# Optimization experiments

Hardware: AMD Instinct MI355X
Metric: run time of the kernel (lower is better)

## Reference

```python
import jax, jax.numpy as jnp
import numpy as np

N = 20000
E = 320000
IN_CH = 512
OUT_CH = 256


def setup_inputs() -> dict:
    key = jax.random.key(0)
    ks = jax.random.split(key, 24)
    p = lambda k, shape: jax.random.normal(k, shape, jnp.float32) * 0.05
    return {
        "x": jax.random.normal(ks[0], (N, IN_CH), jnp.float32),
        "edge_index": jax.random.randint(ks[1], (2, E), 0, N),
        "original_size": 16384,
        "W1": p(ks[2], (IN_CH, 4 * 256)), "as1": p(ks[3], (4, 256)), "ad1": p(ks[4], (4, 256)), "b1": p(ks[5], (1024,)),
        "lw1": p(ks[6], (IN_CH, 1024)), "lb1": p(ks[7], (1024,)),
        "W2": p(ks[8], (1024, 4 * 256)), "as2": p(ks[9], (4, 256)), "ad2": p(ks[10], (4, 256)), "b2": p(ks[11], (1024,)),
        "lw2": p(ks[12], (1024, 1024)), "lb2": p(ks[13], (1024,)),
        "W3": p(ks[14], (1024, 6 * 256)), "as3": p(ks[15], (6, 256)), "ad3": p(ks[16], (6, 256)), "b3": p(ks[17], (256,)),
        "lw3": p(ks[18], (1024, OUT_CH)), "lb3": p(ks[19], (OUT_CH,)),
    }


def gat_conv(x, src, dst, W, a_src, a_dst, bias, heads, ch, concat):
    """PyG-style GATConv: gather -> edge attention -> segment softmax -> scatter-add."""
    n = x.shape[0]
    h = (x @ W).reshape(n, heads, ch)                      # [N,H,C]
    alpha_s = (h * a_src[None]).sum(-1)                    # [N,H]
    alpha_d = (h * a_dst[None]).sum(-1)                    # [N,H]
    e = jax.nn.leaky_relu(alpha_s[src] + alpha_d[dst], 0.2)  # [E,H]
    m = jax.ops.segment_max(e, dst, num_segments=n)        # per-dst max (stable softmax)
    e = jnp.exp(e - m[dst])
    denom = jax.ops.segment_sum(e, dst, num_segments=n)
    alpha = e / (denom[dst] + 1e-16)                       # [E,H]
    msg = h[src] * alpha[:, :, None]                       # [E,H,C]
    out = jax.ops.segment_sum(msg, dst, num_segments=n)    # [N,H,C]
    out = out.reshape(n, heads * ch) if concat else out.mean(axis=1)
    return out + bias


def reference(x, edge_index, original_size, W1, as1, ad1, b1, lw1, lb1,
              W2, as2, ad2, b2, lw2, lb2, W3, as3, ad3, b3, lw3, lb3):
    n = x.shape[0]
    loops = jnp.arange(n)
    src = jnp.concatenate([edge_index[0], loops])  # PyG add_self_loops=True default
    dst = jnp.concatenate([edge_index[1], loops])
    h = jax.nn.elu(gat_conv(x, src, dst, W1, as1, ad1, b1, 4, 256, True) + x @ lw1 + lb1)
    h = jax.nn.elu(gat_conv(h, src, dst, W2, as2, ad2, b2, 4, 256, True) + h @ lw2 + lb2)
    h = gat_conv(h, src, dst, W3, as3, ad3, b3, 6, 256, False) + h @ lw3 + lb3
    return h[:original_size]
```

## Files before the change

kernel.cpp:

```cpp
#include <hip/hip_runtime.h>

#define N_NODES 20000
#define M_PAD   20096
#define E_EDGES 320000

typedef unsigned short u16;
typedef unsigned int   u32;
typedef __attribute__((ext_vector_type(8))) short bf16x8;
typedef __attribute__((ext_vector_type(4))) float f32x4;
typedef __attribute__((ext_vector_type(4))) u32   u32x4;

__device__ __forceinline__ float bf2f(u16 u){
  u32 x = ((u32)u) << 16; float f; __builtin_memcpy(&f, &x, 4); return f;
}
__device__ __forceinline__ u16 f2bf(float f){
  u32 u; __builtin_memcpy(&u, &f, 4);
  u += 0x7fffu + ((u >> 16) & 1u);
  return (u16)(u >> 16);
}
__device__ __forceinline__ float lrelu(float x){ return x > 0.f ? x : 0.2f * x; }

__device__ __forceinline__ void gl_lds16(const void* g, void* l){
  __builtin_amdgcn_global_load_lds((const __attribute__((address_space(1))) void*)g,
                                   (__attribute__((address_space(3))) void*)l, 16, 0, 0);
}

__device__ __forceinline__ void acc8(float* acc, float w, u32x4 p){
#pragma unroll
  for (int d = 0; d < 4; d++){
    u32 u = p[d];
    acc[2 * d]     += w * bf2f((u16)(u & 0xffff));
    acc[2 * d + 1] += w * bf2f((u16)(u >> 16));
  }
}

__device__ __forceinline__ void acc24(float* acc, float w0, float w1, int bnd,
                                      u32x4 p0, u32x4 p1, u32x4 p2){
  u32 u[12];
  *(u32x4*)(u) = p0; *(u32x4*)(u + 4) = p1; *(u32x4*)(u + 8) = p2;
#pragma unroll
  for (int d = 0; d < 12; d++){
    float w = (2 * d < bnd) ? w0 : w1;
    acc[2 * d]     += w * bf2f((u16)(u[d] & 0xffff));
    acc[2 * d + 1] += w * bf2f((u16)(u[d] >> 16));
  }
}

__device__ __forceinline__ float sel6(const float* a, int h){
  float r = a[0];
  r = (h == 1) ? a[1] : r; r = (h == 2) ? a[2] : r; r = (h == 3) ? a[3] : r;
  r = (h == 4) ? a[4] : r; r = (h == 5) ? a[5] : r;
  return r;
}

__global__ void hist_k(const int* __restrict__ ei, int* __restrict__ cnt){
  int i = blockIdx.x * 256 + threadIdx.x;
  if (i < E_EDGES) atomicAdd(&cnt[ei[E_EDGES + i]], 1);
}

__global__ void scan_k(const int* __restrict__ cnt, int* __restrict__ rowp,
                       int* __restrict__ fill, int n){
  __shared__ int wsum[16], wpre[16];
  __shared__ int carry;
  int tid = threadIdx.x, lane = tid & 63, wv = tid >> 6;
  if (tid == 0) carry = 0;
  __syncthreads();
  for (int base = 0; base < n; base += 1024){
    int i = base + tid;
    int v = (i < n) ? cnt[i] : 0;
    int incl = v;
#pragma unroll
    for (int d = 1; d < 64; d <<= 1){
      int t = __shfl_up(incl, d, 64);
      if (lane >= d) incl += t;
    }
    if (lane == 63) wsum[wv] = incl;
    __syncthreads();
    if (tid == 0){
      int s = carry;
#pragma unroll
      for (int w = 0; w < 16; w++){ wpre[w] = s; s += wsum[w]; }
      carry = s;
    }
    __syncthreads();
    if (i < n){ int e = wpre[wv] + incl - v; rowp[i] = e; fill[i] = e; }
  }
  __syncthreads();
  if (tid == 0) rowp[n] = carry;
}

__global__ void scatter_k(const int* __restrict__ ei, int* __restrict__ fill, int* __restrict__ esrc){
  int i = blockIdx.x * 256 + threadIdx.x;
  if (i < E_EDGES){
    int d = ei[E_EDGES + i];
    int p = atomicAdd(&fill[d], 1);
    esrc[p] = ei[i];
  }
}

__global__ void tcast_all(const float* __restrict__ W1, const float* __restrict__ lw1, u16* __restrict__ Wt1,
                          const float* __restrict__ W2, const float* __restrict__ lw2, u16* __restrict__ Wt2,
                          const float* __restrict__ W3, const float* __restrict__ lw3, u16* __restrict__ Wt3)
{
  __shared__ float tile[32][33];
  int b = blockIdx.x;
  const float* src; u16* dst; int Nc, n0, ldd;
  if      (b <  512){            src = W1;  Nc = 1024; dst = Wt1; n0 = 0;    ldd = 512;  }
  else if (b < 1024){ b -=  512; src = lw1; Nc = 1024; dst = Wt1; n0 = 1024; ldd = 512;  }
  else if (b < 2048){ b -= 1024; src = W2;  Nc = 1024; dst = Wt2; n0 = 0;    ldd = 1024; }
  else if (b < 3072){ b -= 2048; src = lw2; Nc = 1024; dst = Wt2; n0 = 1024; ldd = 1024; }
  else if (b < 4608){ b -= 3072; src = W3;  Nc = 1536; dst = Wt3; n0 = 0;    ldd = 1024; }
  else              { b -= 4608; src = lw3; Nc = 256;  dst = Wt3; n0 = 1536; ldd = 1024; }
  int gx = Nc / 32;
  int kb = (b / gx) * 32, nb = (b % gx) * 32;
  int tx = threadIdx.x, ty = threadIdx.y;
#pragma unroll
  for (int r = 0; r < 32; r += 8)
    tile[ty + r][tx] = src[(size_t)(kb + ty + r) * Nc + nb + tx];
  __syncthreads();
#pragma unroll
  for (int r = 0; r < 32; r += 8){
    int n = nb + ty + r;
    dst[(size_t)(n0 + n) * ldd + kb + tx] = f2bf(tile[tx][ty + r]);
  }
}

__global__ void castx_k(const float* __restrict__ x, u16* __restrict__ o, int realRows){
  int r = blockIdx.x, c = threadIdx.x * 2;
  float2 v = (r < realRows) ? *(const float2*)(x + (size_t)r * 512 + c) : make_float2(0.f, 0.f);
  u32 pk = ((u32)f2bf(v.y) << 16) | (u32)f2bf(v.x);
  *(u32*)(o + (size_t)r * 512 + c) = pk;
}

__global__ void zpad_k(u16* __restrict__ p, int n){
  int i = blockIdx.x * 256 + threadIdx.x; if (i < n) p[i] = 0;
}

__global__ __launch_bounds__(256, 2)
void gemm_bf16(const u16* __restrict__ A, const u16* __restrict__ Bt, u16* __restrict__ C,
               int N, int K,
               const float* __restrict__ a_s, const float* __restrict__ a_d,
               float* __restrict__ aS, float* __restrict__ aD, int H)
{
  __shared__ __attribute__((aligned(16))) u16 lA[128 * 32];
  __shared__ __attribute__((aligned(16))) u16 lB[256 * 32];
  const int tid  = threadIdx.x;
  const int wave = tid >> 6, lane = tid & 63;
  const int bn = blockIdx.x, bm = blockIdx.y;
  const int wm = (wave >> 1) * 64, wn = (wave & 1) * 128;

  const int srow  = wave * 16 + (lane >> 2);
  const int skcol = (lane & 3) * 8;
  const u16* Ag0 = A  + (size_t)(bm * 128 + srow) * K + skcol;
  const u16* Ag1 = Ag0 + (size_t)64 * K;
  const u16* Bg  = Bt + (size_t)(bn * 256 + srow) * K + skcol;
  u16* lA0 = lA + wave * 512; u16* lA1 = lA + 2048 + wave * 512;
  u16* lBw = lB + wave * 512;

  f32x4 acc[4][8] = {};

  for (int k0 = 0; k0 < K; k0 += 32){
    gl_lds16(Ag0 + k0, lA0);
    gl_lds16(Ag1 + k0, lA1);
#pragma unroll
    for (int c = 0; c < 4; c++)
      gl_lds16(Bg + (size_t)(c * 64) * K + k0, lBw + c * 2048);
    __syncthreads();
    const int koff = (lane >> 4) * 8;
    const int rsel = lane & 15;
    bf16x8 af[4], bfr[8];
#pragma unroll
    for (int i = 0; i < 4; i++) af[i]  = *(const bf16x8*)&lA[(wm + i * 16 + rsel) * 32 + koff];
#pragma unroll
    for (int j = 0; j < 8; j++) bfr[j] = *(const bf16x8*)&lB[(wn + j * 16 + rsel) * 32 + koff];
#pragma unroll
    for (int i = 0; i < 4; i++)
#pragma unroll
      for (int j = 0; j < 8; j++)
        acc[i][j] = __builtin_amdgcn_mfma_f32_16x16x32_bf16(af[i], bfr[j], acc[i][j], 0, 0, 0);
    __syncthreads();
  }

  const int r0 = (lane >> 4) * 4, cl = lane & 15;
#pragma unroll
  for (int i = 0; i < 4; i++)
#pragma unroll
    for (int j = 0; j < 8; j++){
      int row = bm * 128 + wm + i * 16 + r0;
      int col = bn * 256 + wn + j * 16 + cl;
      u16* cp = C + (size_t)row * N + col;
#pragma unroll
      for (int r = 0; r < 4; r++) cp[(size_t)r * N] = f2bf(acc[i][j][r]);
    }

  if (bn < H){
    float* fa = (float*)lA;
    fa[tid]       = a_s[bn * 256 + tid];
    fa[256 + tid] = a_d[bn * 256 + tid];
    __syncthreads();
    float* fb = (float*)lB;
    const int q = lane >> 4;
#pragma unroll
    for (int i = 0; i < 4; i++)
#pragma unroll
      for (int r = 0; r < 4; r++){
        float ps = 0.f, pd = 0.f;
#pragma unroll
        for (int j = 0; j < 8; j++){
          float v = acc[i][j][r];
          int c = wn + j * 16 + cl;
          ps += v * fa[c];
          pd += v * fa[256 + c];
        }
#pragma unroll
        for (int m = 1; m < 16; m <<= 1){
          ps += __shfl_xor(ps, m, 64);
          pd += __shfl_xor(pd, m, 64);
        }
        if (cl == 0){
          int row = wm + i * 16 + q * 4 + r;
          fb[(wave & 1) * 128 + row]       = ps;
          fb[256 + (wave & 1) * 128 + row] = pd;
        }
      }
    __syncthreads();
    if (tid < 128){
      int row = bm * 128 + tid;
      aS[(size_t)row * 8 + bn] = fb[tid] + fb[128 + tid];
      aD[(size_t)row * 8 + bn] = fb[256 + tid] + fb[384 + tid];
    }
  }
}

__global__ __launch_bounds__(256)
void agg4w_k(const u16* __restrict__ HG, int ldH,
             const int* __restrict__ rowp, const int* __restrict__ esrc,
             const float* __restrict__ aS, const float* __restrict__ aD,
             const float* __restrict__ bias, const float* __restrict__ lbias,
             u16* __restrict__ outb)
{
  __shared__ float s_w[4][256];
  const int tid = threadIdx.x, lane = tid & 63, wv = tid >> 6;
  const int dst = blockIdx.x * 4 + wv;
  const int e0 = rowp[dst];
  const int deg = rowp[dst + 1] - e0;
  const int nE = deg + 1;
  const float4 adv = *(const float4*)(aD + (size_t)dst * 8);

  int myS = dst;
  float ea = -1e30f, eb = -1e30f, ec = -1e30f, ed = -1e30f;
  if (lane < nE){
    myS = (lane == deg) ? dst : esrc[e0 + lane];
    float4 as = *(const float4*)(aS + (size_t)myS * 8);
    ea = lrelu(as.x + adv.x); eb = lrelu(as.y + adv.y);
    ec = lrelu(as.z + adv.z); ed = lrelu(as.w + adv.w);
  }
  float m0 = ea, m1 = eb, m2 = ec, m3 = ed;
  for (int i = lane + 64; i < nE; i += 64){
    int s = (i == deg) ? dst : esrc[e0 + i];
    float4 as = *(const float4*)(aS + (size_t)s * 8);
    m0 = fmaxf(m0, lrelu(as.x + adv.x)); m1 = fmaxf(m1, lrelu(as.y + adv.y));
    m2 = fmaxf(m2, lrelu(as.z + adv.z)); m3 = fmaxf(m3, lrelu(as.w + adv.w));
  }
#pragma unroll
  for (int off = 1; off < 64; off <<= 1){
    m0 = fmaxf(m0, __shfl_xor(m0, off)); m1 = fmaxf(m1, __shfl_xor(m1, off));
    m2 = fmaxf(m2, __shfl_xor(m2, off)); m3 = fmaxf(m3, __shfl_xor(m3, off));
  }

  float w0 = __expf(ea - m0), w1 = __expf(eb - m1);
  float w2 = __expf(ec - m2), w3 = __expf(ed - m3);
  float l0 = w0, l1 = w1, l2 = w2, l3 = w3;
  for (int i = lane + 64; i < nE; i += 64){
    int s = (i == deg) ? dst : esrc[e0 + i];
    float4 as = *(const float4*)(aS + (size_t)s * 8);
    l0 += __expf(lrelu(as.x + adv.x) - m0); l1 += __expf(lrelu(as.y + adv.y) - m1);
    l2 += __expf(lrelu(as.z + adv.z) - m2); l3 += __expf(lrelu(as.w + adv.w) - m3);
  }
#pragma unroll
  for (int off = 1; off < 64; off <<= 1){
    l0 += __shfl_xor(l0, off); l1 += __shfl_xor(l1, off);
    l2 += __shfl_xor(l2, off); l3 += __shfl_xor(l3, off);
  }
  float d0 = 1.f / (l0 + 1e-16f), d1 = 1.f / (l1 + 1e-16f);
  float d2 = 1.f / (l2 + 1e-16f), d3 = 1.f / (l3 + 1e-16f);
  *(float4*)&s_w[wv][lane * 4] = make_float4(w0 * d0, w1 * d1, w2 * d2, w3 * d3);
  __syncthreads();

  const int h = lane >> 4;
  const int ch0 = lane * 16;
  const float mh   = (h < 2) ? (h == 0 ? m0 : m1) : (h == 2 ? m2 : m3);
  const float dh   = (h < 2) ? (h == 0 ? d0 : d1) : (h == 2 ? d2 : d3);
  const float advh = (h < 2) ? (h == 0 ? adv.x : adv.y) : (h == 2 ? adv.z : adv.w);
  float acc[16] = {};
  const u16* HGc = HG + ch0;
  const int nF = nE < 64 ? nE : 64;
  int i = 0;
  for (; i + 1 < nF; i += 2){
    int sA = __shfl(myS, i), sB = __shfl(myS, i + 1);
    float wA = s_w[wv][i * 4 + h], wB = s_w[wv][(i + 1) * 4 + h];
    const u16* ra = HGc + (size_t)sA * ldH;
    const u16* rb = HGc + (size_t)sB * ldH;
    u32x4 pa0 = *(const u32x4*)ra, pa1 = *(const u32x4*)(ra + 8);
    u32x4 pb0 = *(const u32x4*)rb, pb1 = *(const u32x4*)(rb + 8);
    acc8(acc, wA, pa0); acc8(acc + 8, wA, pa1);
    acc8(acc, wB, pb0); acc8(acc + 8, wB, pb1);
  }
  if (i < nF){
    int sA = __shfl(myS, i);
    float wA = s_w[wv][i * 4 + h];
    const u16* ra = HGc + (size_t)sA * ldH;
    acc8(acc, wA, *(const u32x4*)ra); acc8(acc + 8, wA, *(const u32x4*)(ra + 8));
  }
  for (int j = 64; j < nE; j++){
    int s = (j == deg) ? dst : esrc[e0 + j];
    float e = lrelu(aS[(size_t)s * 8 + h] + advh);
    float w = __expf(e - mh) * dh;
    const u16* r = HGc + (size_t)s * ldH;
    acc8(acc, w, *(const u32x4*)r); acc8(acc + 8, w, *(const u32x4*)(r + 8));
  }

  const u16* lr = HG + (size_t)dst * ldH + 1024 + ch0;
  u32x4 q0 = *(const u32x4*)lr, q1 = *(const u32x4*)(lr + 8);
  float lin[16];
#pragma unroll
  for (int d = 0; d < 4; d++){
    lin[2*d]     = bf2f((u16)(q0[d] & 0xffff)); lin[2*d+1]   = bf2f((u16)(q0[d] >> 16));
    lin[8+2*d]   = bf2f((u16)(q1[d] & 0xffff)); lin[8+2*d+1] = bf2f((u16)(q1[d] >> 16));
  }
  u32 o[8];
#pragma unroll
  for (int d = 0; d < 8; d++){
    float va = acc[2*d]   + bias[ch0 + 2*d]   + lin[2*d]   + lbias[ch0 + 2*d];
    float vb = acc[2*d+1] + bias[ch0 + 2*d+1] + lin[2*d+1] + lbias[ch0 + 2*d+1];
    va = va > 0.f ? va : __expf(va) - 1.f;
    vb = vb > 0.f ? vb : __expf(vb) - 1.f;
    o[d] = ((u32)f2bf(vb) << 16) | (u32)f2bf(va);
  }
  u16* op = outb + (size_t)dst * 1024 + ch0;
  *(u32x4*)op = *(u32x4*)o;
  *(u32x4*)(op + 8) = *(u32x4*)(o + 4);
}

__global__ __launch_bounds__(256)
void agg6w_k(const u16* __restrict__ HG, int ldH,
             const int* __restrict__ rowp, const int* __restrict__ esrc,
             const float* __restrict__ aS, const float* __restrict__ aD,
             const float* __restrict__ bias, const float* __restrict__ lbias,
             float* __restrict__ outf)
{
  __shared__ float s_w[4][64 * 6];
  __shared__ float s_fin[4][1536];
  const int tid = threadIdx.x, lane = tid & 63, wv = tid >> 6;
  const int dst = blockIdx.x * 4 + wv;
  const int e0 = rowp[dst];
  const int deg = rowp[dst + 1] - e0;
  const int nE = deg + 1;

  const float* advp = aD + (size_t)dst * 8;
  float4 av4 = *(const float4*)advp; float2 av2 = *(const float2*)(advp + 4);
  float adv[6] = { av4.x, av4.y, av4.z, av4.w, av2.x, av2.y };

  int myS = dst;
  float e[6];
#pragma unroll
  for (int h = 0; h < 6; h++) e[h] = -1e30f;
  if (lane < nE){
    myS = (lane == deg) ? dst : esrc[e0 + lane];
    float4 a0 = *(const float4*)(aS + (size_t)myS * 8);
    float2 a1 = *(const float2*)(aS + (size_t)myS * 8 + 4);
    e[0] = lrelu(a0.x + adv[0]); e[1] = lrelu(a0.y + adv[1]);
    e[2] = lrelu(a0.z + adv[2]); e[3] = lrelu(a0.w + adv[3]);
    e[4] = lrelu(a1.x + adv[4]); e[5] = lrelu(a1.y + adv[5]);
  }
  float m[6];
#pragma unroll
  for (int h = 0; h < 6; h++) m[h] = e[h];
  for (int i = lane + 64; i < nE; i += 64){
    int s = (i == deg) ? dst : esrc[e0 + i];
    float4 a0 = *(const float4*)(aS + (size_t)s * 8);
    float2 a1 = *(const float2*)(aS + (size_t)s * 8 + 4);
    float t[6] = { a0.x, a0.y, a0.z, a0.w, a1.x, a1.y };
#pragma unroll
    for (int h = 0; h < 6; h++) m[h] = fmaxf(m[h], lrelu(t[h] + adv[h]));
  }
#pragma unroll
  for (int h = 0; h < 6; h++)
#pragma unroll
    for (int off = 1; off < 64; off <<= 1) m[h] = fmaxf(m[h], __shfl_xor(m[h], off));

  float w[6], l[6];
#pragma unroll
  for (int h = 0; h < 6; h++){ w[h] = __expf(e[h] - m[h]); l[h] = w[h]; }
  for (int i = lane + 64; i < nE; i += 64){
    int s = (i == deg) ? dst : esrc[e0 + i];
    float4 a0 = *(const float4*)(aS + (size_t)s * 8);
    float2 a1 = *(const float2*)(aS + (size_t)s * 8 + 4);
    float t[6] = { a0.x, a0.y, a0.z, a0.w, a1.x, a1.y };
#pragma unroll
    for (int h = 0; h < 6; h++) l[h] += __expf(lrelu(t[h] + adv[h]) - m[h]);
  }
#pragma unroll
  for (int h = 0; h < 6; h++)
#pragma unroll
    for (int off = 1; off < 64; off <<= 1) l[h] += __shfl_xor(l[h], off);
  float dv[6];
#pragma unroll
  for (int h = 0; h < 6; h++) dv[h] = 1.f / (l[h] + 1e-16f);
  float* swp = &s_w[wv][lane * 6];
  ((float2*)swp)[0] = make_float2(w[0] * dv[0], w[1] * dv[1]);
  ((float2*)swp)[1] = make_float2(w[2] * dv[2], w[3] * dv[3]);
  ((float2*)swp)[2] = make_float2(w[4] * dv[4], w[5] * dv[5]);
  __syncthreads();

  const int ch0 = lane * 24;
  const int h0 = ch0 >> 8, h1 = (ch0 + 23) >> 8;
  const int bnd = (h0 + 1) * 256 - ch0;
  const float mh0 = sel6(m, h0), mh1 = sel6(m, h1);
  const float dh0 = sel6(dv, h0), dh1 = sel6(dv, h1);
  const float ah0 = sel6(adv, h0), ah1 = sel6(adv, h1);
  float acc[24] = {};
  const u16* HGc = HG + ch0;
  const int nF = nE < 64 ? nE : 64;
  for (int i = 0; i < nF; i++){
    int s = __shfl(myS, i);
    float wA0 = s_w[wv][i * 6 + h0], wA1 = s_w[wv][i * 6 + h1];
    const u16* r = HGc + (size_t)s * ldH;
    acc24(acc, wA0, wA1, bnd,
          *(const u32x4*)r, *(const u32x4*)(r + 8), *(const u32x4*)(r + 16));
  }
  for (int j = 64; j < nE; j++){
    int s = (j == deg) ? dst : esrc[e0 + j];
    float w0 = __expf(lrelu(aS[(size_t)s * 8 + h0] + ah0) - mh0) * dh0;
    float w1 = __expf(lrelu(aS[(size_t)s * 8 + h1] + ah1) - mh1) * dh1;
    const u16* r = HGc + (size_t)s * ldH;
    acc24(acc, w0, w1, bnd,
          *(const u32x4*)r, *(const u32x4*)(r + 8), *(const u32x4*)(r + 16));
  }
#pragma unroll
  for (int d = 0; d < 6; d++)
    *(float4*)&s_fin[wv][ch0 + d * 4] = make_float4(acc[4*d], acc[4*d+1], acc[4*d+2], acc[4*d+3]);
  __syncthreads();

  const int c0 = lane * 4;
  float4 sum = make_float4(0.f, 0.f, 0.f, 0.f);
#pragma unroll
  for (int h = 0; h < 6; h++){
    float4 t = *(const float4*)&s_fin[wv][h * 256 + c0];
    sum.x += t.x; sum.y += t.y; sum.z += t.z; sum.w += t.w;
  }
  ushort4 uq = *(const ushort4*)(HG + (size_t)dst * ldH + 1536 + c0);
  float4 bv = *(const float4*)(bias + c0);
  float4 lb = *(const float4*)(lbias + c0);
  float4 o;
  o.x = sum.x * (1.f/6.f) + bv.x + bf2f(uq.x) + lb.x;
  o.y = sum.y * (1.f/6.f) + bv.y + bf2f(uq.y) + lb.y;
  o.z = sum.z * (1.f/6.f) + bv.z + bf2f(uq.z) + lb.z;
  o.w = sum.w * (1.f/6.f) + bv.w + bf2f(uq.w) + lb.w;
  *(float4*)(outf + (size_t)dst * 256 + c0) = o;
}

extern "C" void kernel_launch(void* const* d_in, const int* in_sizes, int n_in,
                              void* d_out, int out_size, void* d_ws, size_t ws_size,
                              hipStream_t stream)
{
  const float* x   = (const float*)d_in[0];
  const int*   ei  = (const int*)  d_in[1];
  const float* W1  = (const float*)d_in[3];
  const float* as1 = (const float*)d_in[4];
  const float* ad1 = (const float*)d_in[5];
  const float* b1  = (const float*)d_in[6];
  const float* lw1 = (const float*)d_in[7];
  const float* lb1 = (const float*)d_in[8];
  const float* W2  = (const float*)d_in[9];
  const float* as2 = (const float*)d_in[10];
  const float* ad2 = (const float*)d_in[11];
  const float* b2  = (const float*)d_in[12];
  const float* lb2p= (const float*)d_in[14];
  const float* lw2 = (const float*)d_in[13];
  const float* W3  = (const float*)d_in[15];
  const float* as3 = (const float*)d_in[16];
  const float* ad3 = (const float*)d_in[17];
  const float* b3  = (const float*)d_in[18];
  const float* lw3 = (const float*)d_in[19];
  const float* lb3 = (const float*)d_in[20];

  char* wp = (char*)d_ws;
  auto nxt = [&](size_t b) -> void* {
    void* p = (void*)wp; wp += (b + 255) & ~(size_t)255; return p;
  };
  u16*  Wt1  = (u16*) nxt((size_t)2048 * 512  * 2);
  u16*  Wt2  = (u16*) nxt((size_t)2048 * 1024 * 2);
  u16*  Wt3  = (u16*) nxt((size_t)1792 * 1024 * 2);
  u16*  Xb   = (u16*) nxt((size_t)M_PAD * 1024 * 2);
  u16*  HG   = (u16*) nxt((size_t)M_PAD * 2048 * 2);
  float* aS  = (float*)nxt((size_t)M_PAD * 8 * 4);
  float* aD  = (float*)nxt((size_t)M_PAD * 8 * 4);
  int*  cnt  = (int*)  nxt((size_t)N_NODES * 4);
  int*  rowp = (int*)  nxt((size_t)(N_NODES + 1) * 4);
  int*  fill = (int*)  nxt((size_t)N_NODES * 4);
  int*  esrc = (int*)  nxt((size_t)E_EDGES * 4);

  hipMemsetAsync(cnt, 0, (size_t)N_NODES * 4, stream);
  hist_k   <<<(E_EDGES + 255) / 256, 256, 0, stream>>>(ei, cnt);
  scan_k   <<<1, 1024, 0, stream>>>(cnt, rowp, fill, N_NODES);
  scatter_k<<<(E_EDGES + 255) / 256, 256, 0, stream>>>(ei, fill, esrc);

  tcast_all<<<4864, dim3(32, 8), 0, stream>>>(W1, lw1, Wt1, W2, lw2, Wt2, W3, lw3, Wt3);

  castx_k<<<M_PAD, 256, 0, stream>>>(x, Xb, N_NODES);
  zpad_k <<<(96 * 1024 + 255) / 256, 256, 0, stream>>>(Xb + (size_t)N_NODES * 1024, 96 * 1024);

  const int MT = M_PAD / 128;

  gemm_bf16<<<dim3(2048 / 256, MT), 256, 0, stream>>>(Xb, Wt1, HG, 2048, 512,  as1, ad1, aS, aD, 4);
  agg4w_k  <<<N_NODES / 4, 256, 0, stream>>>(HG, 2048, rowp, esrc, aS, aD, b1, lb1, Xb);

  gemm_bf16<<<dim3(2048 / 256, MT), 256, 0, stream>>>(Xb, Wt2, HG, 2048, 1024, as2, ad2, aS, aD, 4);
  agg4w_k  <<<N_NODES / 4, 256, 0, stream>>>(HG, 2048, rowp, esrc, aS, aD, b2, lb2p, Xb);

  gemm_bf16<<<dim3(1792 / 256, MT), 256, 0, stream>>>(Xb, Wt3, HG, 1792, 1024, as3, ad3, aS, aD, 6);
  int outRows = out_size / 256;
  agg6w_k  <<<outRows / 4, 256, 0, stream>>>(HG, 1792, rowp, esrc, aS, aD, b3, lb3, (float*)d_out);

  (void)in_sizes; (void)n_in; (void)ws_size;
}
```

Measured before the change: 865.2 us.

## Restructure layer-3 aggregation to per-lane 8 channels across heads, unroll layer-1/2 gather by 4

The 6-head aggregation kernel now assigns each lane 8 output channels and has it accumulate all 6 heads directly, with the two half-waves splitting the edges and combining through a cross-half shuffle. The head mean is folded into the softmax normalisation. This removes the shared-memory head-reduction buffer, its extra barrier and the per-lane head-boundary selection logic. The 4-head aggregation loop is also unrolled to four edges per iteration so more gather loads are in flight at once. The cost is more loads per edge per lane in layer 3 and more register pressure in the unrolled loop.

```diff
diff --git a/kernel.cpp b/kernel.cpp
--- a/kernel.cpp
+++ b/kernel.cpp
@@ -32,25 +32,6 @@
     acc[2 * d]     += w * bf2f((u16)(u & 0xffff));
     acc[2 * d + 1] += w * bf2f((u16)(u >> 16));
   }
-}
-
-__device__ __forceinline__ void acc24(float* acc, float w0, float w1, int bnd,
-                                      u32x4 p0, u32x4 p1, u32x4 p2){
-  u32 u[12];
-  *(u32x4*)(u) = p0; *(u32x4*)(u + 4) = p1; *(u32x4*)(u + 8) = p2;
-#pragma unroll
-  for (int d = 0; d < 12; d++){
-    float w = (2 * d < bnd) ? w0 : w1;
-    acc[2 * d]     += w * bf2f((u16)(u[d] & 0xffff));
-    acc[2 * d + 1] += w * bf2f((u16)(u[d] >> 16));
-  }
-}
-
-__device__ __forceinline__ float sel6(const float* a, int h){
-  float r = a[0];
-  r = (h == 1) ? a[1] : r; r = (h == 2) ? a[2] : r; r = (h == 3) ? a[3] : r;
-  r = (h == 4) ? a[4] : r; r = (h == 5) ? a[5] : r;
-  return r;
 }
 
 __global__ void hist_k(const int* __restrict__ ei, int* __restrict__ cnt){
@@ -296,17 +277,25 @@
   const u16* HGc = HG + ch0;
   const int nF = nE < 64 ? nE : 64;
   int i = 0;
-  for (; i + 1 < nF; i += 2){
-    int sA = __shfl(myS, i), sB = __shfl(myS, i + 1);
-    float wA = s_w[wv][i * 4 + h], wB = s_w[wv][(i + 1) * 4 + h];
+  for (; i + 3 < nF; i += 4){
+    int sA = __shfl(myS, i),     sB = __shfl(myS, i + 1);
+    int sC = __shfl(myS, i + 2), sD = __shfl(myS, i + 3);
+    float wA = s_w[wv][i * 4 + h],       wB = s_w[wv][(i + 1) * 4 + h];
+    float wC = s_w[wv][(i + 2) * 4 + h], wD = s_w[wv][(i + 3) * 4 + h];
     const u16* ra = HGc + (size_t)sA * ldH;
     const u16* rb = HGc + (size_t)sB * ldH;
+    const u16* rc = HGc + (size_t)sC * ldH;
+    const u16* rd = HGc + (size_t)sD * ldH;
     u32x4 pa0 = *(const u32x4*)ra, pa1 = *(const u32x4*)(ra + 8);
     u32x4 pb0 = *(const u32x4*)rb, pb1 = *(const u32x4*)(rb + 8);
+    u32x4 pc0 = *(const u32x4*)rc, pc1 = *(const u32x4*)(rc + 8);
+    u32x4 pd0 = *(const u32x4*)rd, pd1 = *(const u32x4*)(rd + 8);
     acc8(acc, wA, pa0); acc8(acc + 8, wA, pa1);
     acc8(acc, wB, pb0); acc8(acc + 8, wB, pb1);
-  }
-  if (i < nF){
+    acc8(acc, wC, pc0); acc8(acc + 8, wC, pc1);
+    acc8(acc, wD, pd0); acc8(acc + 8, wD, pd1);
+  }
+  for (; i < nF; i++){
     int sA = __shfl(myS, i);
     float wA = s_w[wv][i * 4 + h];
     const u16* ra = HGc + (size_t)sA * ldH;
@@ -350,7 +339,6 @@
              float* __restrict__ outf)
 {
   __shared__ float s_w[4][64 * 6];
-  __shared__ float s_fin[4][1536];
   const int tid = threadIdx.x, lane = tid & 63, wv = tid >> 6;
   const int dst = blockIdx.x * 4 + wv;
   const int e0 = rowp[dst];
@@ -406,58 +394,63 @@
     for (int off = 1; off < 64; off <<= 1) l[h] += __shfl_xor(l[h], off);
   float dv[6];
 #pragma unroll
-  for (int h = 0; h < 6; h++) dv[h] = 1.f / (l[h] + 1e-16f);
+  for (int h = 0; h < 6; h++) dv[h] = (1.f / 6.f) / (l[h] + 1e-16f);
   float* swp = &s_w[wv][lane * 6];
   ((float2*)swp)[0] = make_float2(w[0] * dv[0], w[1] * dv[1]);
   ((float2*)swp)[1] = make_float2(w[2] * dv[2], w[3] * dv[3]);
   ((float2*)swp)[2] = make_float2(w[4] * dv[4], w[5] * dv[5]);
   __syncthreads();
 
-  const int ch0 = lane * 24;
-  const int h0 = ch0 >> 8, h1 = (ch0 + 23) >> 8;
-  const int bnd = (h0 + 1) * 256 - ch0;
-  const float mh0 = sel6(m, h0), mh1 = sel6(m, h1);
-  const float dh0 = sel6(dv, h0), dh1 = sel6(dv, h1);
-  const float ah0 = sel6(adv, h0), ah1 = sel6(adv, h1);
-  float acc[24] = {};
+  const int li = lane & 31, half = lane >> 5;
+  const int ch0 = li * 8;
+  float acc[8] = {};
   const u16* HGc = HG + ch0;
   const int nF = nE < 64 ? nE : 64;
-  for (int i = 0; i < nF; i++){
+  for (int i = half; i < nF; i += 2){
     int s = __shfl(myS, i);
-    float wA0 = s_w[wv][i * 6 + h0], wA1 = s_w[wv][i * 6 + h1];
     const u16* r = HGc + (size_t)s * ldH;
-    acc24(acc, wA0, wA1, bnd,
-          *(const u32x4*)r, *(const u32x4*)(r + 8), *(const u32x4*)(r + 16));
-  }
-  for (int j = 64; j < nE; j++){
+    const float* wp6 = &s_w[wv][i * 6];
+#pragma unroll
+    for (int h = 0; h < 6; h++){
+      u32x4 p = *(const u32x4*)(r + h * 256);
+      acc8(acc, wp6[h], p);
+    }
+  }
+  for (int j = 64 + half; j < nE; j += 2){
     int s = (j == deg) ? dst : esrc[e0 + j];
-    float w0 = __expf(lrelu(aS[(size_t)s * 8 + h0] + ah0) - mh0) * dh0;
-    float w1 = __expf(lrelu(aS[(size_t)s * 8 + h1] + ah1) - mh1) * dh1;
+    float4 a0 = *(const float4*)(aS + (size_t)s * 8);
+    float2 a1 = *(const float2*)(aS + (size_t)s * 8 + 4);
+    float t[6] = { a0.x, a0.y, a0.z, a0.w, a1.x, a1.y };
     const u16* r = HGc + (size_t)s * ldH;
-    acc24(acc, w0, w1, bnd,
-          *(const u32x4*)r, *(const u32x4*)(r + 8), *(const u32x4*)(r + 16));
-  }
-#pragma unroll
-  for (int d = 0; d < 6; d++)
-    *(float4*)&s_fin[wv][ch0 + d * 4] = make_float4(acc[4*d], acc[4*d+1], acc[4*d+2], acc[4*d+3]);
-  __syncthreads();
-
-  const int c0 = lane * 4;
-  float4 sum = make_float4(0.f, 0.f, 0.f, 0.f);
-#pragma unroll
-  for (int h = 0; h < 6; h++){
-    float4 t = *(const float4*)&s_fin[wv][h * 256 + c0];
-    sum.x += t.x; sum.y += t.y; sum.z += t.z; sum.w += t.w;
-  }
-  ushort4 uq = *(const ushort4*)(HG + (size_t)dst * ldH + 1536 + c0);
-  float4 bv = *(const float4*)(bias + c0);
-  float4 lb = *(const float4*)(lbias + c0);
-  float4 o;
-  o.x = sum.x * (1.f/6.f) + bv.x + bf2f(uq.x) + lb.x;
-  o.y = sum.y * (1.f/6.f) + bv.y + bf2f(uq.y) + lb.y;
-  o.z = sum.z * (1.f/6.f) + bv.z + bf2f(uq.z) + lb.z;
-  o.w = sum.w * (1.f/6.f) + bv.w + bf2f(uq.w) + lb.w;
-  *(float4*)(outf + (size_t)dst * 256 + c0) = o;
+#pragma unroll
+    for (int h = 0; h < 6; h++){
+      float wt = __expf(lrelu(t[h] + adv[h]) - m[h]) * dv[h];
+      u32x4 p = *(const u32x4*)(r + h * 256);
+      acc8(acc, wt, p);
+    }
+  }
+#pragma unroll
+  for (int c = 0; c < 8; c++) acc[c] += __shfl_xor(acc[c], 32);
+
+  if (lane < 32){
+    u32x4 q = *(const u32x4*)(HG + (size_t)dst * ldH + 1536 + ch0);
+    float lin[8];
+#pragma unroll
+    for (int d = 0; d < 4; d++){
+      lin[2*d]   = bf2f((u16)(q[d] & 0xffff));
+      lin[2*d+1] = bf2f((u16)(q[d] >> 16));
+    }
+    float4 b0 = *(const float4*)(bias + ch0),  b1 = *(const float4*)(bias + ch0 + 4);
+    float4 c0 = *(const float4*)(lbias + ch0), c1 = *(const float4*)(lbias + ch0 + 4);
+    float4 o0, o1;
+    o0.x = acc[0] + b0.x + lin[0] + c0.x; o0.y = acc[1] + b0.y + lin[1] + c0.y;
+    o0.z = acc[2] + b0.z + lin[2] + c0.z; o0.w = acc[3] + b0.w + lin[3] + c0.w;
+    o1.x = acc[4] + b1.x + lin[4] + c1.x; o1.y = acc[5] + b1.y + lin[5] + c1.y;
+    o1.z = acc[6] + b1.z + lin[6] + c1.z; o1.w = acc[7] + b1.w + lin[7] + c1.w;
+    float* op = outf + (size_t)dst * 256 + ch0;
+    *(float4*)op = o0;
+    *(float4*)(op + 4) = o1;
+  }
 }
 
 extern "C" void kernel_launch(void* const* d_in, const int* in_sizes, int n_in,
@@ -476,8 +469,8 @@
   const float* as2 = (const float*)d_in[10];
   const float* ad2 = (const float*)d_in[11];
   const float* b2  = (const float*)d_in[12];
-  const float* lb2p= (const float*)d_in[14];
   const float* lw2 = (const float*)d_in[13];
+  const float* lb2 = (const float*)d_in[14];
   const float* W3  = (const float*)d_in[15];
   const float* as3 = (const float*)d_in[16];
   const float* ad3 = (const float*)d_in[17];
@@ -517,7 +510,7 @@
   agg4w_k  <<<N_NODES / 4, 256, 0, stream>>>(HG, 2048, rowp, esrc, aS, aD, b1, lb1, Xb);
 
   gemm_bf16<<<dim3(2048 / 256, MT), 256, 0, stream>>>(Xb, Wt2, HG, 2048, 1024, as2, ad2, aS, aD, 4);
-  agg4w_k  <<<N_NODES / 4, 256, 0, stream>>>(HG, 2048, rowp, esrc, aS, aD, b2, lb2p, Xb);
+  agg4w_k  <<<N_NODES / 4, 256, 0, stream>>>(HG, 2048, rowp, esrc, aS, aD, b2, lb2, Xb);
 
   gemm_bf16<<<dim3(1792 / 256, MT), 256, 0, stream>>>(Xb, Wt3, HG, 1792, 1024, as3, ad3, aS, aD, 6);
   int outRows = out_size / 256;
```

Measured after the change: 840.9 us. 1.03x faster.
